# Performance work log

Measured on AMD Instinct MI355X. Metric: run time of the kernel, lower is better.

The kernel has to match this reference:

```python
import jax, jax.numpy as jnp
import numpy as np

BS, S, D, N, E = 16, 8, 10, 32, 300
H, STATE_DIM, MID, OC = 128, 96, 256, 100

def setup_inputs():
    ks = jax.random.split(jax.random.key(0), 24)
    g = lambda i, shape: (0.02 * jax.random.normal(ks[i], shape)).astype(jnp.float32)
    return {
        "stock_news": jax.random.normal(ks[0], (BS, S, D, N, E), dtype=jnp.float32),
        "stock_feats": jax.random.normal(ks[1], (BS, STATE_DIM), dtype=jnp.float32),
        "conv_w3": g(2, (S, OC, E, 3)), "conv_b3": g(3, (S, OC)),
        "conv_w4": g(4, (S, OC, E, 4)), "conv_b4": g(5, (S, OC)),
        "conv_w5": g(6, (S, OC, E, 5)), "conv_b5": g(7, (S, OC)),
        "w_ih": g(8, (S, 4 * H, 3 * OC)), "w_hh": g(9, (S, 4 * H, H)),
        "b_ih": g(10, (S, 4 * H)), "b_hh": g(11, (S, 4 * H)),
        "linX_w": g(12, (S, H, 2 * H)), "linX_b": g(13, (S, H)),
        "linY_w": g(14, (S, 64, H)), "linY_b": g(15, (S, 64)),
        "w1": g(16, (24, STATE_DIM)), "b1": g(17, (24,)),
        "w2": g(18, (16, 24)), "b2": g(19, (16,)),
        "arch_w1": g(20, (MID, 16 + 64 * S)), "arch_b1": g(21, (MID,)),
        "arch_w2": g(22, (S, MID)), "arch_b2": g(23, (S,)),
        "action_var": jnp.full((S,), -0.25, dtype=jnp.float32),
    }

def _conv_maxpool(x, w, b, k):
    # x: [S,B,D,N,E], w: [S,OC,E,k] -> conv1d over news axis then max-pool -> [S,B,D,OC]
    L = x.shape[3] - k + 1
    y = jnp.broadcast_to(b[:, None, None, None, :], (x.shape[0], x.shape[1], x.shape[2], L, w.shape[1]))
    for j in range(k):
        y = y + jnp.einsum('sbdne,soe->sbdno', x[:, :, :, j:j + L, :], w[:, :, :, j])
    return y.max(axis=3)

def _lstm_attn(xs, w_ih, w_hh, b_ih, b_hh):
    # single-stock LSTM (batch_first) + attention from original code; xs: [B,D,I] -> [B,2H]
    pre = jnp.einsum('bdi,gi->dbg', xs, w_ih) + b_ih + b_hh  # [D,B,4H]
    h0 = jnp.zeros((xs.shape[0], w_hh.shape[1]), xs.dtype)
    def step(carry, g_t):
        h, c = carry
        gates = g_t + h @ w_hh.T
        i, f, g, o = jnp.split(gates, 4, axis=-1)  # PyTorch gate order i,f,g,o
        c = jax.nn.sigmoid(f) * c + jax.nn.sigmoid(i) * jnp.tanh(g)
        h = jax.nn.sigmoid(o) * jnp.tanh(c)
        return (h, c), h
    (hn, _), outs = jax.lax.scan(step, (h0, h0), pre)
    outs = outs.transpose(1, 0, 2)  # [B,D,H]
    w = jnp.einsum('bh,bdh->bd', hn, outs)[:, None, :]  # [B,1,D]
    w = jax.nn.softmax(w, axis=1)  # softmax over singleton dim, exactly as torch code (yields ones)
    out = jnp.sum(w.transpose(0, 2, 1) * outs, axis=1)  # [B,H]
    return jnp.concatenate([hn, out], axis=-1)  # [B,2H]

def _forward(stock_news, stock_feats, conv_w3, conv_b3, conv_w4, conv_b4, conv_w5, conv_b5,
             w_ih, w_hh, b_ih, b_hh, linX_w, linX_b, linY_w, linY_b,
             w1, b1, w2, b2, arch_w1, arch_b1, arch_w2, arch_b2, action_var):
    x = stock_news.transpose(1, 0, 2, 3, 4)  # [S,B,D,N,E]
    feats = [_conv_maxpool(x, w, b, k) for (w, b, k) in
             ((conv_w3, conv_b3, 3), (conv_w4, conv_b4, 4), (conv_w5, conv_b5, 5))]
    text = jnp.concatenate(feats, axis=-1)  # [S,B,D,300]
    comb = jax.vmap(_lstm_attn)(text, w_ih, w_hh, b_ih, b_hh)  # [S,B,2H]
    hX = jax.nn.relu(jnp.einsum('sbi,shi->sbh', comb, linX_w) + linX_b[:, None, :])  # dropout is eval-mode identity
    hY = jax.nn.relu(jnp.einsum('sbh,soh->sbo', hX, linY_w) + linY_b[:, None, :])  # [S,B,64]
    stock_text = hY.transpose(1, 0, 2).reshape(stock_news.shape[0], -1)  # [B,S*64]
    f = jax.nn.relu(stock_feats @ w1.T + b1) @ w2.T + b2  # [B,16]
    total = jnp.concatenate([stock_text, f], axis=-1)  # [B,16+64S]
    mu = jnp.tanh(jax.nn.relu(total @ arch_w1.T + arch_b1) @ arch_w2.T + arch_b2)
    return mu, jnp.exp(action_var)

def reference(stock_news, stock_feats, conv_w3, conv_b3, conv_w4, conv_b4, conv_w5, conv_b5,
              w_ih, w_hh, b_ih, b_hh, linX_w, linX_b, linY_w, linY_b,
              w1, b1, w2, b2, arch_w1, arch_b1, arch_w2, arch_b2, action_var):
    return _forward(stock_news, stock_feats, conv_w3, conv_b3, conv_w4, conv_b4, conv_w5, conv_b5,
                    w_ih, w_hh, b_ih, b_hh, linX_w, linX_b, linY_w, linY_b,
                    w1, b1, w2, b2, arch_w1, arch_b1, arch_w2, arch_b2, action_var)
```

## Files before the change

kernel.cpp:

```cpp
#include <hip/hip_runtime.h>
#include <math.h>

#define S_   8
#define B_   16
#define D_   10
#define N_   32
#define E_   300
#define H_   128
#define G4_  512
#define SDIM_ 96
#define MID_ 256
#define TOT_ 528

typedef unsigned short u16;
typedef unsigned int u32;
typedef __attribute__((ext_vector_type(8))) short short8;
typedef __attribute__((ext_vector_type(4))) short short4v;
typedef __attribute__((ext_vector_type(4))) float f32x4;

static __device__ __forceinline__ u16 f2bf(float f) {
    unsigned u = __builtin_bit_cast(unsigned, f);
    return (u16)((u + 0x7FFFu + ((u >> 16) & 1u)) >> 16);
}

__global__ __launch_bounds__(256) void prep(
        const float* __restrict__ w3, const float* __restrict__ b3,
        const float* __restrict__ w4, const float* __restrict__ b4,
        const float* __restrict__ w5, const float* __restrict__ b5,
        const float* __restrict__ w_ih,
        const float* __restrict__ lxw, const float* __restrict__ lyw,
        const float* __restrict__ aw1,
        u16* __restrict__ wpack2, u16* __restrict__ wpre2,
        float* __restrict__ bcomb,
        float* __restrict__ lxwT, float* __restrict__ lywT,
        float* __restrict__ aw1T) {
    const int blk = blockIdx.x, tid = threadIdx.x;

    if (blk < 160) {
        __shared__ u16 tile[16][1504];
        const int s = blk / 20, cg = blk % 20;
        for (int i = tid; i < 16 * 752; i += 256)
            reinterpret_cast<u32*>(&tile[0][0])[i] = 0u;
        __syncthreads();
        const int ch = tid >> 4, lane = tid & 15;
        const int c = cg * 16 + ch;
        const float* src = nullptr; int cnt = 0, ktap = 3;
        if (c < 100)      { src = w3 + (size_t)((s * 100 + c      ) * 300) * 3; cnt = 900;  ktap = 3; }
        else if (c < 200) { src = w4 + (size_t)((s * 100 + c - 100) * 300) * 4; cnt = 1200; ktap = 4; }
        else if (c < 300) { src = w5 + (size_t)((s * 100 + c - 200) * 300) * 5; cnt = 1500; ktap = 5; }
        for (int p = lane; p < cnt; p += 16) {
            int e = p / ktap, tap = p - e * ktap;
            tile[ch][tap * 300 + e] = f2bf(src[p]);
        }
        __syncthreads();
        u32* dst0 = reinterpret_cast<u32*>(wpack2 + (size_t)s * 481280 + cg * 512);
        const int mch = tid >> 4, rem = (tid * 2) & 31;
        for (int ks = 0; ks < 47; ++ks) {
            u32 v = (u32)tile[mch][ks * 32 + rem] | ((u32)tile[mch][ks * 32 + rem + 1] << 16);
            dst0[(size_t)ks * 5120 + tid] = v;
        }
    } else if (blk < 416) {
        __shared__ u16 tile2[16][320];
        const int u = blk - 160, s = u >> 5, gg = u & 31;
        const int ch = tid >> 4, lane = tid & 15;
        const int g = gg * 16 + ch;
        const float* src = w_ih + (size_t)(s * 512 + g) * 300;
        for (int p = lane; p < 320; p += 16)
            tile2[ch][p] = (p < 300) ? f2bf(src[p]) : (u16)0;
        __syncthreads();
        u32* dst0 = reinterpret_cast<u32*>(wpre2 + (size_t)s * 163840 + gg * 512);
        const int mch = tid >> 4, rem = (tid * 2) & 31;
        for (int ks = 0; ks < 10; ++ks) {
            u32 v = (u32)tile2[mch][ks * 32 + rem] | ((u32)tile2[mch][ks * 32 + rem + 1] << 16);
            dst0[(size_t)ks * 8192 + tid] = v;
        }
    } else if (blk < 872) {
        __shared__ float ldsT[32][33];
        const float* inp; float* outp;
        int inRS, outRS, i0, t0, ivalid = 32;
        if (blk < 672) {
            int u = blk - 416, s = u >> 5, t32 = u & 31;
            int it = t32 >> 2, tt = t32 & 3;
            inp = lxw + (size_t)s * 128 * 256; outp = lxwT + (size_t)s * 256 * 128;
            inRS = 256; outRS = 128; i0 = it * 32; t0 = tt * 32;
        } else if (blk < 736) {
            int u = blk - 672, s = u >> 3, t32 = u & 7;
            int it = t32 >> 1, tt = t32 & 1;
            inp = lyw + (size_t)s * 64 * 128; outp = lywT + (size_t)s * 128 * 64;
            inRS = 128; outRS = 64; i0 = it * 32; t0 = tt * 32;
        } else {
            int u = blk - 736;
            int it = u >> 3, jt = u & 7;
            inp = aw1; outp = aw1T;
            inRS = 528; outRS = 256; i0 = it * 32; t0 = jt * 32;
            ivalid = (i0 + 32 <= 528) ? 32 : (528 - i0);
        }
        const int row = tid >> 3, cf = tid & 7;
        float4 v = make_float4(0.f, 0.f, 0.f, 0.f);
        if (cf * 4 < ivalid)
            v = *reinterpret_cast<const float4*>(inp + (size_t)(t0 + row) * inRS + i0 + cf * 4);
        ldsT[cf * 4 + 0][row] = v.x; ldsT[cf * 4 + 1][row] = v.y;
        ldsT[cf * 4 + 2][row] = v.z; ldsT[cf * 4 + 3][row] = v.w;
        __syncthreads();
        if (row < ivalid) {
            float4 w;
            w.x = ldsT[row][cf * 4 + 0]; w.y = ldsT[row][cf * 4 + 1];
            w.z = ldsT[row][cf * 4 + 2]; w.w = ldsT[row][cf * 4 + 3];
            *reinterpret_cast<float4*>(outp + (size_t)(i0 + row) * outRS + t0 + cf * 4) = w;
        }
    } else {
        for (int i = tid; i < 2560; i += 256) {
            int c = i % 320, s = i / 320;
            float bv = 0.f;
            if (c < 100)      bv = b3[s*100 + c];
            else if (c < 200) bv = b4[s*100 + c - 100];
            else if (c < 300) bv = b5[s*100 + c - 200];
            bcomb[i] = bv;
        }
    }
}

__global__ __launch_bounds__(512, 1) void conv_mfma(const float* __restrict__ news,
                                                    const u16* __restrict__ wpack2,
                                                    const float* __restrict__ bcomb,
                                                    u16* __restrict__ text_bf) {
    __shared__ u16 xs[5 * 10816];
    __shared__ float part[10][320];
    const int tid = threadIdx.x, bid = blockIdx.x;
    const int s = bid & 7, rr_ = bid >> 3, b = rr_ >> 1, half = rr_ & 1;
    const int l = tid & 63, wvi = tid >> 6;
    const int wm = wvi >> 2, wn = wvi & 3;
    const int q = l >> 4, r16 = l & 15;

    const u16* gp[5];
#pragma unroll
    for (int nt = 0; nt < 5; ++nt) {
        int c = wn * 80 + nt * 16 + r16;
        gp[nt] = wpack2 + (size_t)s * 481280 + c * 32 + q * 8;
    }

    short8 bf0[5], bf1[5];
#pragma unroll
    for (int nt = 0; nt < 5; ++nt) bf0[nt] = *reinterpret_cast<const short8*>(gp[nt]);
#pragma unroll
    for (int nt = 0; nt < 5; ++nt) bf1[nt] = *reinterpret_cast<const short8*>(gp[nt] + 10240);

    {
        const float4* xg = reinterpret_cast<const float4*>(
            news + (size_t)((b * 8 + s) * 10 + half * 5) * 9600);
        for (int base = 0; base < 12000; base += 4096) {
            float4 v[8];
#pragma unroll
            for (int j = 0; j < 8; ++j) {
                int idx = base + j * 512 + tid;
                if (idx < 12000) v[j] = xg[idx];
            }
#pragma unroll
            for (int j = 0; j < 8; ++j) {
                int idx = base + j * 512 + tid;
                if (idx < 12000) {
                    int day = idx / 2400, rem = idx - day * 2400;
                    ushort4 o;
                    o.x = f2bf(v[j].x); o.y = f2bf(v[j].y);
                    o.z = f2bf(v[j].z); o.w = f2bf(v[j].w);
                    *reinterpret_cast<ushort4*>(&xs[day * 10816 + rem * 4]) = o;
                }
            }
        }
        for (int i = tid; i < 1520; i += 512) {
            int day = i / 304, p = i - day * 304;
            *reinterpret_cast<unsigned*>(&xs[day * 10816 + 9600 + p * 2]) = 0u;
        }
    }
    __syncthreads();

    f32x4 acc[5][5];
#pragma unroll
    for (int mt = 0; mt < 5; ++mt)
#pragma unroll
        for (int nt = 0; nt < 5; ++nt) acc[mt][nt] = (f32x4)(0.f);

#define LOADA(dst, ks) do {                                                       \
    _Pragma("unroll")                                                             \
    for (int mt_ = 0; mt_ < 5; ++mt_) {                                           \
        int di_ = wm * 5 + mt_;                                                   \
        int off_ = (di_ >> 1) * 10816 + (((di_ & 1) << 4) + r16) * 300            \
                   + (ks) * 32 + q * 8;                                           \
        short4v lo_ = *reinterpret_cast<const short4v*>(&xs[off_]);               \
        short4v hi_ = *reinterpret_cast<const short4v*>(&xs[off_ + 4]);           \
        dst[mt_] = __builtin_shufflevector(lo_, hi_, 0, 1, 2, 3, 4, 5, 6, 7);     \
    } } while (0)

#define MFMAS(bfv, av) do {                                                       \
    _Pragma("unroll")                                                             \
    for (int nt_ = 0; nt_ < 5; ++nt_)                                             \
        _Pragma("unroll")                                                         \
        for (int mt_ = 0; mt_ < 5; ++mt_)                                         \
            acc[mt_][nt_] = __builtin_amdgcn_mfma_f32_16x16x32_bf16(av[mt_], bfv[nt_], acc[mt_][nt_], 0, 0, 0); \
    } while (0)

    for (int ks = 0; ks < 46; ks += 2) {
        short8 a0[5], a1[5];
        LOADA(a0, ks);
        MFMAS(bf0, a0);
#pragma unroll
        for (int nt = 0; nt < 5; ++nt)
            bf0[nt] = *reinterpret_cast<const short8*>(gp[nt] + (ks + 2) * 10240);

        LOADA(a1, ks + 1);
        MFMAS(bf1, a1);
        if (ks + 3 < 47) {
#pragma unroll
            for (int nt = 0; nt < 5; ++nt)
                bf1[nt] = *reinterpret_cast<const short8*>(gp[nt] + (ks + 3) * 10240);
        }
    }
    {
        short8 a0[5];
        LOADA(a0, 46);
        MFMAS(bf0, a0);
    }
#undef LOADA
#undef MFMAS

#pragma unroll
    for (int mt = 0; mt < 5; ++mt) {
        const int di = wm * 5 + mt;
        const int nwb = (di & 1) << 4;
#pragma unroll
        for (int nt = 0; nt < 5; ++nt) {
            int oc = wn * 80 + nt * 16 + r16;
            int L = (oc < 100) ? 30 : (oc < 200) ? 29 : 28;
            float mx = -3e38f;
#pragma unroll
            for (int rr = 0; rr < 4; ++rr) {
                int nw = nwb + q * 4 + rr;
                if (nw < L) mx = fmaxf(mx, acc[mt][nt][rr]);
            }
            mx = fmaxf(mx, __shfl_xor(mx, 16));
            mx = fmaxf(mx, __shfl_xor(mx, 32));
            if (l < 16) part[di][wn * 80 + nt * 16 + l] = mx;
        }
    }
    __syncthreads();
    for (int i = tid; i < 1600; i += 512) {
        int day = i / 320, oc = i - day * 320;
        float mx = fmaxf(part[2 * day][oc], part[2 * day + 1][oc]);
        text_bf[((size_t)(s * 16 + b) * 10 + half * 5 + day) * 320 + oc] =
            f2bf(mx + bcomb[s * 320 + oc]);
    }
}

__global__ __launch_bounds__(256) void lstm_pre_mfma(const u16* __restrict__ text_bf,
                                                     const u16* __restrict__ wpre2,
                                                     const float* __restrict__ b_ih,
                                                     const float* __restrict__ b_hh,
                                                     float* __restrict__ pre) {
    __shared__ u16 as16[16 * 320];
    const int sd = blockIdx.x, s = sd / 10, d = sd % 10;
    const int tid = threadIdx.x, l = tid & 63, w = tid >> 6, q = l >> 4, r16 = l & 15;

    for (int i = tid; i < 640; i += 256) {
        int r = i / 40, c = i % 40;
        *reinterpret_cast<float4*>(as16 + r * 320 + ((c ^ (r & 7)) << 3)) =
            *reinterpret_cast<const float4*>(text_bf + ((size_t)(s * 16 + r) * 10 + d) * 320 + c * 8);
    }
    __syncthreads();

    const u16* gpb[8];
#pragma unroll
    for (int nt = 0; nt < 8; ++nt) {
        int g = w * 128 + nt * 16 + r16;
        gpb[nt] = wpre2 + (size_t)s * 163840 + g * 32 + q * 8;
    }

    f32x4 acc[8];
#pragma unroll
    for (int nt = 0; nt < 8; ++nt) acc[nt] = (f32x4)(0.f);

    for (int ks = 0; ks < 10; ++ks) {
        short8 a = *reinterpret_cast<const short8*>(
            as16 + r16 * 320 + (((ks * 4 + q) ^ (r16 & 7)) << 3));
#pragma unroll
        for (int nt = 0; nt < 8; ++nt) {
            short8 bf = *reinterpret_cast<const short8*>(gpb[nt] + ks * 16384);
            acc[nt] = __builtin_amdgcn_mfma_f32_16x16x32_bf16(a, bf, acc[nt], 0, 0, 0);
        }
    }

#pragma unroll
    for (int nt = 0; nt < 8; ++nt) {
        int g = w * 128 + nt * 16 + r16;
        float bias = b_ih[s * 512 + g] + b_hh[s * 512 + g];
#pragma unroll
        for (int r = 0; r < 4; ++r) {
            int brow = q * 4 + r;
            pre[((size_t)sd * 16 + brow) * 512 + g] = acc[nt][r] + bias;
        }
    }
}

__global__ __launch_bounds__(512) void lstm_tail(const float* __restrict__ pre,
                                                 const float* __restrict__ w_hh,
                                                 const float* __restrict__ lxwT, const float* __restrict__ lxb,
                                                 const float* __restrict__ lywT, const float* __restrict__ lyb,
                                                 float* __restrict__ total) {
    __shared__ float wchunk[128][129];
    __shared__ float h_lds[H_];
    __shared__ float gates[G4_];
    __shared__ float comb_l[256];
    __shared__ __align__(16) float hx[H_];
    const int sb = blockIdx.x;
    const int s = sb / B_, b = sb % B_;
    const int t = threadIdx.x;

    float wrs[128];
    for (int c = 0; c < 4; ++c) {
        for (int i2 = t; i2 < 128 * 32; i2 += 512) {
            int row = i2 >> 5, fq = i2 & 31;
            float4 v = *reinterpret_cast<const float4*>(
                w_hh + ((size_t)(s * G4_ + c * 128 + row)) * H_ + fq * 4);
            wchunk[row][fq * 4 + 0] = v.x; wchunk[row][fq * 4 + 1] = v.y;
            wchunk[row][fq * 4 + 2] = v.z; wchunk[row][fq * 4 + 3] = v.w;
        }
        __syncthreads();
        if ((t >> 7) == c) {
            int r = t & 127;
#pragma unroll
            for (int i = 0; i < 128; ++i) wrs[i] = wchunk[r][i];
        }
        __syncthreads();
    }

    float cc = 0.f, hsum = 0.f, hval = 0.f;
    if (t < H_) h_lds[t] = 0.f;
    __syncthreads();

    for (int d = 0; d < D_; ++d) {
        float a0 = pre[(((size_t)(s * D_ + d) * B_ + b)) * G4_ + t];
        float a1 = 0.f, a2 = 0.f, a3 = 0.f;
#pragma unroll
        for (int i = 0; i < 128; i += 4) {
            float4 h4 = *reinterpret_cast<const float4*>(&h_lds[i]);
            a0 = fmaf(wrs[i + 0], h4.x, a0);
            a1 = fmaf(wrs[i + 1], h4.y, a1);
            a2 = fmaf(wrs[i + 2], h4.z, a2);
            a3 = fmaf(wrs[i + 3], h4.w, a3);
        }
        gates[t] = (a0 + a1) + (a2 + a3);
        __syncthreads();
        if (t < H_) {
            float ig = 1.f / (1.f + expf(-gates[t]));
            float fg = 1.f / (1.f + expf(-gates[H_ + t]));
            float gg = tanhf(gates[2 * H_ + t]);
            float og = 1.f / (1.f + expf(-gates[3 * H_ + t]));
            cc = fg * cc + ig * gg;
            hval = og * tanhf(cc);
            hsum += hval;
            h_lds[t] = hval;
        }
        __syncthreads();
    }
    if (t < H_) { comb_l[t] = hval; comb_l[H_ + t] = hsum; }
    __syncthreads();
    if (t < H_) {
        const float* wv = lxwT + (size_t)s * 256 * 128 + t;
        float a0 = lxb[s * H_ + t], a1 = 0.f;
        for (int i = 0; i < 256; i += 2) {
            a0 = fmaf(comb_l[i], wv[(size_t)i * 128], a0);
            a1 = fmaf(comb_l[i + 1], wv[(size_t)(i + 1) * 128], a1);
        }
        hx[t] = fmaxf(a0 + a1, 0.f);
    }
    __syncthreads();
    if (t < 64) {
        const float* wv = lywT + (size_t)s * 128 * 64 + t;
        float a0 = lyb[s * 64 + t], a1 = 0.f;
        for (int i = 0; i < 128; i += 2) {
            a0 = fmaf(hx[i], wv[(size_t)i * 64], a0);
            a1 = fmaf(hx[i + 1], wv[(size_t)(i + 1) * 64], a1);
        }
        total[(size_t)b * 512 + s * 64 + t] = fmaxf(a0 + a1, 0.f);
    }
}

__global__ __launch_bounds__(512) void head_feats(const float* __restrict__ total,
                                                  const float* __restrict__ sf,
                                                  const float* __restrict__ w1, const float* __restrict__ b1,
                                                  const float* __restrict__ w2, const float* __restrict__ b2,
                                                  const float* __restrict__ aw1T, const float* __restrict__ ab1,
                                                  const float* __restrict__ aw2, const float* __restrict__ ab2,
                                                  const float* __restrict__ avar,
                                                  float* __restrict__ out) {
    __shared__ __align__(16) float tr[TOT_];
    __shared__ float hid[MID_];
    __shared__ float h1f[24];
    __shared__ float pA[MID_], pB[MID_];
    const int bb = blockIdx.x, t = threadIdx.x;
    if (t < 128)
        reinterpret_cast<float4*>(tr)[t] = reinterpret_cast<const float4*>(total + (size_t)bb * 512)[t];
    if (t < 24) {
        float acc = b1[t];
        for (int i = 0; i < SDIM_; ++i) acc = fmaf(sf[bb * SDIM_ + i], w1[t * SDIM_ + i], acc);
        h1f[t] = fmaxf(acc, 0.f);
    }
    __syncthreads();
    if (t < 16) {
        float acc = b2[t];
        for (int i = 0; i < 24; ++i) acc = fmaf(h1f[i], w2[t * 24 + i], acc);
        tr[512 + t] = acc;
    }
    __syncthreads();
    {
        const int j = t & 255, hf = t >> 8;
        const int ilo = hf ? 264 : 0, ihi = hf ? 528 : 264;
        const float* wv = aw1T + j;
        float a0 = 0.f, a1 = 0.f, a2 = 0.f, a3 = 0.f;
        for (int i = ilo; i < ihi; i += 4) {
            a0 = fmaf(tr[i + 0], wv[(size_t)(i + 0) * 256], a0);
            a1 = fmaf(tr[i + 1], wv[(size_t)(i + 1) * 256], a1);
            a2 = fmaf(tr[i + 2], wv[(size_t)(i + 2) * 256], a2);
            a3 = fmaf(tr[i + 3], wv[(size_t)(i + 3) * 256], a3);
        }
        float p = (a0 + a1) + (a2 + a3);
        if (hf) pB[j] = p; else pA[j] = p;
    }
    __syncthreads();
    if (t < MID_) hid[t] = fmaxf(pA[t] + pB[t] + ab1[t], 0.f);
    __syncthreads();
    if (t < 8) {
        float acc = ab2[t];
        const float* wv = aw2 + (size_t)t * MID_;
        for (int i = 0; i < MID_; ++i) acc = fmaf(hid[i], wv[i], acc);
        out[bb * 8 + t] = tanhf(acc);
    }
    if (bb == 0 && t >= 8 && t < 16) out[128 + (t - 8)] = expf(avar[t - 8]);
}

extern "C" void kernel_launch(void* const* d_in, const int* in_sizes, int n_in,
                              void* d_out, int out_size, void* d_ws, size_t ws_size,
                              hipStream_t stream) {
    const float* news = (const float*)d_in[0];
    const float* sf   = (const float*)d_in[1];
    const float* w3   = (const float*)d_in[2];  const float* b3 = (const float*)d_in[3];
    const float* w4   = (const float*)d_in[4];  const float* b4 = (const float*)d_in[5];
    const float* w5   = (const float*)d_in[6];  const float* b5 = (const float*)d_in[7];
    const float* w_ih = (const float*)d_in[8];  const float* w_hh = (const float*)d_in[9];
    const float* b_ih = (const float*)d_in[10]; const float* b_hh = (const float*)d_in[11];
    const float* lxw  = (const float*)d_in[12]; const float* lxb = (const float*)d_in[13];
    const float* lyw  = (const float*)d_in[14]; const float* lyb = (const float*)d_in[15];
    const float* w1   = (const float*)d_in[16]; const float* b1 = (const float*)d_in[17];
    const float* w2   = (const float*)d_in[18]; const float* b2 = (const float*)d_in[19];
    const float* aw1  = (const float*)d_in[20]; const float* ab1 = (const float*)d_in[21];
    const float* aw2  = (const float*)d_in[22]; const float* ab2 = (const float*)d_in[23];
    const float* avar = (const float*)d_in[24];

    char* ws = (char*)d_ws;
    u16*   wpack2  = (u16*)ws;
    u16*   wpre2   = (u16*)(ws + 7700480);
    float* bcomb   = (float*)(ws + 10321920);
    u16*   text_bf = (u16*)(ws + 10332160);
    float* pre     = (float*)(ws + 11151360);
    float* total   = (float*)(ws + 13772800);
    float* lxwT    = (float*)(ws + 13805568);
    float* lywT    = (float*)(ws + 14854144);
    float* aw1T    = (float*)(ws + 15116288);

    prep<<<873, 256, 0, stream>>>(w3, b3, w4, b4, w5, b5, w_ih, lxw, lyw, aw1,
                                  wpack2, wpre2, bcomb, lxwT, lywT, aw1T);
    conv_mfma<<<256, 512, 0, stream>>>(news, wpack2, bcomb, text_bf);
    lstm_pre_mfma<<<S_ * D_, 256, 0, stream>>>(text_bf, wpre2, b_ih, b_hh, pre);
    lstm_tail<<<S_ * B_, 512, 0, stream>>>(pre, w_hh, lxwT, lxb, lywT, lyb, total);
    head_feats<<<B_, 512, 0, stream>>>(total, sf, w1, b1, w2, b2, aw1T, ab1, aw2, ab2, avar, (float*)d_out);
}
```

Measured before the change: 133.0 us.

## Fuse LSTM input projection into the recurrent tail kernel via LDS

Merges the separate LSTM input-projection MFMA kernel into the per-(stock,batch) recurrent kernel. Each block now computes its own 10 time-step gate pre-activations (padded to 16 rows) with MFMA into shared memory, removing one launch and the global write and read of the pre buffer. In exchange the wpre weights are re-read by 128 blocks instead of 80, with each block wasting 6 of 16 MFMA rows, and shared memory use rises by 20KB.

```diff
diff --git a/kernel.cpp b/kernel.cpp
--- a/kernel.cpp
+++ b/kernel.cpp
@@ -251,71 +251,69 @@
     }
 }
 
-__global__ __launch_bounds__(256) void lstm_pre_mfma(const u16* __restrict__ text_bf,
-                                                     const u16* __restrict__ wpre2,
-                                                     const float* __restrict__ b_ih,
-                                                     const float* __restrict__ b_hh,
-                                                     float* __restrict__ pre) {
+__global__ __launch_bounds__(512) void stock_tail(const u16* __restrict__ text_bf,
+                                                  const u16* __restrict__ wpre2,
+                                                  const float* __restrict__ b_ih,
+                                                  const float* __restrict__ b_hh,
+                                                  const float* __restrict__ w_hh,
+                                                  const float* __restrict__ lxwT, const float* __restrict__ lxb,
+                                                  const float* __restrict__ lywT, const float* __restrict__ lyb,
+                                                  float* __restrict__ total) {
     __shared__ u16 as16[16 * 320];
-    const int sd = blockIdx.x, s = sd / 10, d = sd % 10;
-    const int tid = threadIdx.x, l = tid & 63, w = tid >> 6, q = l >> 4, r16 = l & 15;
-
-    for (int i = tid; i < 640; i += 256) {
-        int r = i / 40, c = i % 40;
-        *reinterpret_cast<float4*>(as16 + r * 320 + ((c ^ (r & 7)) << 3)) =
-            *reinterpret_cast<const float4*>(text_bf + ((size_t)(s * 16 + r) * 10 + d) * 320 + c * 8);
-    }
-    __syncthreads();
-
-    const u16* gpb[8];
-#pragma unroll
-    for (int nt = 0; nt < 8; ++nt) {
-        int g = w * 128 + nt * 16 + r16;
-        gpb[nt] = wpre2 + (size_t)s * 163840 + g * 32 + q * 8;
-    }
-
-    f32x4 acc[8];
-#pragma unroll
-    for (int nt = 0; nt < 8; ++nt) acc[nt] = (f32x4)(0.f);
-
-    for (int ks = 0; ks < 10; ++ks) {
-        short8 a = *reinterpret_cast<const short8*>(
-            as16 + r16 * 320 + (((ks * 4 + q) ^ (r16 & 7)) << 3));
-#pragma unroll
-        for (int nt = 0; nt < 8; ++nt) {
-            short8 bf = *reinterpret_cast<const short8*>(gpb[nt] + ks * 16384);
-            acc[nt] = __builtin_amdgcn_mfma_f32_16x16x32_bf16(a, bf, acc[nt], 0, 0, 0);
-        }
-    }
-
-#pragma unroll
-    for (int nt = 0; nt < 8; ++nt) {
-        int g = w * 128 + nt * 16 + r16;
-        float bias = b_ih[s * 512 + g] + b_hh[s * 512 + g];
-#pragma unroll
-        for (int r = 0; r < 4; ++r) {
-            int brow = q * 4 + r;
-            pre[((size_t)sd * 16 + brow) * 512 + g] = acc[nt][r] + bias;
-        }
-    }
-}
-
-__global__ __launch_bounds__(512) void lstm_tail(const float* __restrict__ pre,
-                                                 const float* __restrict__ w_hh,
-                                                 const float* __restrict__ lxwT, const float* __restrict__ lxb,
-                                                 const float* __restrict__ lywT, const float* __restrict__ lyb,
-                                                 float* __restrict__ total) {
+    __shared__ float pre_lds[D_][G4_];
     __shared__ float wchunk[128][129];
     __shared__ float h_lds[H_];
     __shared__ float gates[G4_];
     __shared__ float comb_l[256];
     __shared__ __align__(16) float hx[H_];
     const int sb = blockIdx.x;
-    const int s = sb / B_, b = sb % B_;
-    const int t = threadIdx.x;
+    const int s = sb >> 4, b = sb & 15;
+    const int t = threadIdx.x, l = t & 63, wv = t >> 6, q = l >> 4, r16 = l & 15;
+
+    for (int i = t; i < 640; i += 512) {
+        int r = i / 40, c = i % 40;
+        float4 v = make_float4(0.f, 0.f, 0.f, 0.f);
+        if (r < D_)
+            v = *reinterpret_cast<const float4*>(
+                text_bf + ((size_t)((s * 16 + b) * D_ + r)) * 320 + c * 8);
+        *reinterpret_cast<float4*>(as16 + r * 320 + ((c ^ (r & 7)) << 3)) = v;
+    }
+    __syncthreads();
+
+    {
+        const u16* gpb[4];
+#pragma unroll
+        for (int nt = 0; nt < 4; ++nt) {
+            int g = wv * 64 + nt * 16 + r16;
+            gpb[nt] = wpre2 + (size_t)s * 163840 + g * 32 + q * 8;
+        }
+        f32x4 acc[4];
+#pragma unroll
+        for (int nt = 0; nt < 4; ++nt) acc[nt] = (f32x4)(0.f);
+        for (int ks = 0; ks < 10; ++ks) {
+            short8 a = *reinterpret_cast<const short8*>(
+                as16 + r16 * 320 + (((ks * 4 + q) ^ (r16 & 7)) << 3));
+#pragma unroll
+            for (int nt = 0; nt < 4; ++nt) {
+                short8 bf = *reinterpret_cast<const short8*>(gpb[nt] + ks * 16384);
+                acc[nt] = __builtin_amdgcn_mfma_f32_16x16x32_bf16(a, bf, acc[nt], 0, 0, 0);
+            }
+        }
+#pragma unroll
+        for (int nt = 0; nt < 4; ++nt) {
+            int g = wv * 64 + nt * 16 + r16;
+            float bias = b_ih[s * G4_ + g] + b_hh[s * G4_ + g];
+#pragma unroll
+            for (int rr = 0; rr < 4; ++rr) {
+                int row = q * 4 + rr;
+                if (row < D_) pre_lds[row][g] = acc[nt][rr] + bias;
+            }
+        }
+    }
 
     float wrs[128];
     for (int c = 0; c < 4; ++c) {
+        __syncthreads();
         for (int i2 = t; i2 < 128 * 32; i2 += 512) {
             int row = i2 >> 5, fq = i2 & 31;
             float4 v = *reinterpret_cast<const float4*>(
@@ -329,15 +327,15 @@
 #pragma unroll
             for (int i = 0; i < 128; ++i) wrs[i] = wchunk[r][i];
         }
-        __syncthreads();
-    }
+    }
+    __syncthreads();
 
     float cc = 0.f, hsum = 0.f, hval = 0.f;
     if (t < H_) h_lds[t] = 0.f;
     __syncthreads();
 
     for (int d = 0; d < D_; ++d) {
-        float a0 = pre[(((size_t)(s * D_ + d) * B_ + b)) * G4_ + t];
+        float a0 = pre_lds[d][t];
         float a1 = 0.f, a2 = 0.f, a3 = 0.f;
 #pragma unroll
         for (int i = 0; i < 128; i += 4) {
@@ -364,21 +362,21 @@
     if (t < H_) { comb_l[t] = hval; comb_l[H_ + t] = hsum; }
     __syncthreads();
     if (t < H_) {
-        const float* wv = lxwT + (size_t)s * 256 * 128 + t;
+        const float* wvp = lxwT + (size_t)s * 256 * 128 + t;
         float a0 = lxb[s * H_ + t], a1 = 0.f;
         for (int i = 0; i < 256; i += 2) {
-            a0 = fmaf(comb_l[i], wv[(size_t)i * 128], a0);
-            a1 = fmaf(comb_l[i + 1], wv[(size_t)(i + 1) * 128], a1);
+            a0 = fmaf(comb_l[i], wvp[(size_t)i * 128], a0);
+            a1 = fmaf(comb_l[i + 1], wvp[(size_t)(i + 1) * 128], a1);
         }
         hx[t] = fmaxf(a0 + a1, 0.f);
     }
     __syncthreads();
     if (t < 64) {
-        const float* wv = lywT + (size_t)s * 128 * 64 + t;
+        const float* wvp = lywT + (size_t)s * 128 * 64 + t;
         float a0 = lyb[s * 64 + t], a1 = 0.f;
         for (int i = 0; i < 128; i += 2) {
-            a0 = fmaf(hx[i], wv[(size_t)i * 64], a0);
-            a1 = fmaf(hx[i + 1], wv[(size_t)(i + 1) * 64], a1);
+            a0 = fmaf(hx[i], wvp[(size_t)i * 64], a0);
+            a1 = fmaf(hx[i + 1], wvp[(size_t)(i + 1) * 64], a1);
         }
         total[(size_t)b * 512 + s * 64 + t] = fmaxf(a0 + a1, 0.f);
     }
@@ -460,16 +458,15 @@
     u16*   wpre2   = (u16*)(ws + 7700480);
     float* bcomb   = (float*)(ws + 10321920);
     u16*   text_bf = (u16*)(ws + 10332160);
-    float* pre     = (float*)(ws + 11151360);
-    float* total   = (float*)(ws + 13772800);
-    float* lxwT    = (float*)(ws + 13805568);
-    float* lywT    = (float*)(ws + 14854144);
-    float* aw1T    = (float*)(ws + 15116288);
+    float* total   = (float*)(ws + 11151360);
+    float* lxwT    = (float*)(ws + 11184128);
+    float* lywT    = (float*)(ws + 12232704);
+    float* aw1T    = (float*)(ws + 12494848);
 
     prep<<<873, 256, 0, stream>>>(w3, b3, w4, b4, w5, b5, w_ih, lxw, lyw, aw1,
                                   wpack2, wpre2, bcomb, lxwT, lywT, aw1T);
     conv_mfma<<<256, 512, 0, stream>>>(news, wpack2, bcomb, text_bf);
-    lstm_pre_mfma<<<S_ * D_, 256, 0, stream>>>(text_bf, wpre2, b_ih, b_hh, pre);
-    lstm_tail<<<S_ * B_, 512, 0, stream>>>(pre, w_hh, lxwT, lxb, lywT, lyb, total);
+    stock_tail<<<S_ * B_, 512, 0, stream>>>(text_bf, wpre2, b_ih, b_hh, w_hh,
+                                            lxwT, lxb, lywT, lyb, total);
     head_feats<<<B_, 512, 0, stream>>>(total, sf, w1, b1, w2, b2, aw1T, ab1, aw2, ab2, avar, (float*)d_out);
 }
```

Result: faster. 122.3 us (-8.0%).
